# Performance work log

Measured on AMD Instinct MI355X. Metric: run time of the kernel, lower is better.

Reference implementation:

```python
import jax, jax.numpy as jnp
import numpy as np

N, M = 32768, 1024

def setup_inputs() -> dict:
    key = jax.random.key(0)
    k1, k2, k3, k4, k5 = jax.random.split(key, 5)
    origins = jax.random.normal(k1, (N, 2), dtype=jnp.float32)
    directions = jax.random.normal(k2, (N, 2), dtype=jnp.float32)
    means = jax.random.normal(k3, (M, 4), dtype=jnp.float32)
    # SPD covariances: A @ A^T + I so the inverse is well-defined
    A = jax.random.normal(k4, (M, 4, 4), dtype=jnp.float32) * 0.5
    covariances = jnp.einsum('mij,mkj->mik', A, A) + jnp.eye(4, dtype=jnp.float32)
    labels_embedding = jax.random.normal(k5, (M,), dtype=jnp.float32)
    return {"origins": origins, "directions": directions, "means": means,
            "covariances": covariances, "labels_embedding": labels_embedding}

def reference(origins, directions, means, covariances, labels_embedding):
    pos = jnp.concatenate([origins, directions], axis=1)          # [N,4]
    Sigma_inv = jnp.linalg.inv(covariances)                       # [M,4,4]
    diffs = pos[:, None, :] - means[None, :, :]                   # [N,M,4]
    quad = jnp.einsum('nmd,mde,nme->nm', diffs, Sigma_inv, diffs)  # [N,M]
    pdf = jnp.exp(-0.5 * quad) * labels_embedding[None, :]        # [N,M]
    prob = jax.nn.sigmoid(jnp.sum(pdf, axis=1))                   # [N]
    return prob.reshape(-1, 1)
```

## Files before the change

### kernel.cpp

```cpp
#include <hip/hip_runtime.h>
#include <hip/hip_bf16.h>
#include <math.h>

#define N_RAYS  32768
#define M_GAUSS 1024

typedef short v8s __attribute__((ext_vector_type(8)));
typedef float v4f __attribute__((ext_vector_type(4)));

__device__ __forceinline__ float fexp2(float x) {
#if __has_builtin(__builtin_amdgcn_exp2f)
    return __builtin_amdgcn_exp2f(x);
#else
    return exp2f(x);
#endif
}

union BFU { __hip_bfloat16 b; unsigned short u; };
__device__ __forceinline__ unsigned short f2bf(float f) { BFU x; x.b = __float2bfloat16(f); return x.u; }
__device__ __forceinline__ float bf2f(unsigned short u)  { BFU x; x.u = u; return __bfloat162float(x.b); }

__device__ __forceinline__ void split_bf16(float f, unsigned short& hi, unsigned short& lo) {
    hi = f2bf(f);
    lo = f2bf(f - bf2f(hi));
}

__device__ __forceinline__ void store8(unsigned short* dst, const unsigned short* s) {
    uint4 v;
    v.x = (unsigned)s[0] | ((unsigned)s[1] << 16);
    v.y = (unsigned)s[2] | ((unsigned)s[3] << 16);
    v.z = (unsigned)s[4] | ((unsigned)s[5] << 16);
    v.w = (unsigned)s[6] | ((unsigned)s[7] << 16);
    *reinterpret_cast<uint4*>(dst) = v;
}

__global__ __launch_bounds__(256) void prep_kernel(
    const float*  __restrict__ means,
    const float*  __restrict__ covs,
    unsigned short* __restrict__ Bt)
{
    const int g = blockIdx.x * 256 + threadIdx.x;
    if (g >= M_GAUSS) return;

    const float4* C4 = reinterpret_cast<const float4*>(covs + 16 * g);
    const float4 r0 = C4[0], r1 = C4[1], r2 = C4[2], r3 = C4[3];
    const float a00=r0.x, a01=r0.y, a02=r0.z, a03=r0.w;
    const float a10=r1.x, a11=r1.y, a12=r1.z, a13=r1.w;
    const float a20=r2.x, a21=r2.y, a22=r2.z, a23=r2.w;
    const float a30=r3.x, a31=r3.y, a32=r3.z, a33=r3.w;

    const float s0=a00*a11-a01*a10, s1=a00*a12-a02*a10, s2=a00*a13-a03*a10;
    const float s3=a01*a12-a02*a11, s4=a01*a13-a03*a11, s5=a02*a13-a03*a12;
    const float c5=a22*a33-a23*a32, c4=a21*a33-a23*a31, c3=a21*a32-a22*a31;
    const float c2=a20*a33-a23*a30, c1=a20*a32-a22*a30, c0=a20*a31-a21*a30;
    const float det = s0*c5 - s1*c4 + s2*c3 + s3*c2 - s4*c1 + s5*c0;
    const float id  = 1.0f / det;

    const float b00=( a11*c5 - a12*c4 + a13*c3)*id;
    const float b01=(-a01*c5 + a02*c4 - a03*c3)*id;
    const float b10=(-a10*c5 + a12*c2 - a13*c1)*id;
    const float b11=( a00*c5 - a02*c2 + a03*c1)*id;
    const float b20=( a10*c4 - a11*c2 + a13*c0)*id;
    const float b21=(-a00*c4 + a01*c2 - a03*c0)*id;
    const float b30=(-a10*c3 + a11*c1 - a12*c0)*id;
    const float b31=( a00*c3 - a01*c1 + a02*c0)*id;
    const float b02=( a31*s5 - a32*s4 + a33*s3)*id;
    const float b03=(-a21*s5 + a22*s4 - a23*s3)*id;
    const float b12=(-a30*s5 + a32*s2 - a33*s1)*id;
    const float b13=( a20*s5 - a22*s2 + a23*s1)*id;
    const float b22=( a30*s4 - a31*s2 + a33*s0)*id;
    const float b23=(-a20*s4 + a21*s2 - a23*s0)*id;
    const float b32=(-a30*s3 + a31*s1 - a32*s0)*id;
    const float b33=( a20*s3 - a21*s1 + a22*s0)*id;

    const float m01=0.5f*(b01+b10), m02=0.5f*(b02+b20), m03=0.5f*(b03+b30);
    const float m12=0.5f*(b12+b21), m13=0.5f*(b13+b31), m23=0.5f*(b23+b32);

    const float4 mu = reinterpret_cast<const float4*>(means)[g];
    const float u0=mu.x, u1=mu.y, u2=mu.z, u3=mu.w;
    const float v0 = b00*u0 + m01*u1 + m02*u2 + m03*u3;
    const float v1 = m01*u0 + b11*u1 + m12*u2 + m13*u3;
    const float v2 = m02*u0 + m12*u1 + b22*u2 + m23*u3;
    const float v3 = m03*u0 + m13*u1 + m23*u2 + b33*u3;
    const float cc = u0*v0 + u1*v1 + u2*v2 + u3*v3;

    const float k  = -0.72134752044448170368f;
    const float k2 = 2.0f * k;
    float w[16] = { k*b00,  k*b11,  k*b22,  k*b33,
                    k2*m01, k2*m02, k2*m03, k2*m12, k2*m13, k2*m23,
                    -k2*v0, -k2*v1, -k2*v2, -k2*v3, k*cc, 0.0f };
    unsigned short whi[16], wlo[16];
    #pragma unroll
    for (int q = 0; q < 16; ++q) split_bf16(w[q], whi[q], wlo[q]);

    const int t = g >> 4, cg = g & 15;
    unsigned short* b1 = Bt + (size_t)t * 32 * 8;
    store8(b1 + (0*16 + cg) * 8, whi + 0);
    store8(b1 + (1*16 + cg) * 8, whi + 8);
    unsigned short* b2 = Bt + (size_t)2048 * 8 + (size_t)t * 32 * 8;
    store8(b2 + (0*16 + cg) * 8, wlo + 0);
    store8(b2 + (1*16 + cg) * 8, wlo + 8);
}

__global__ __launch_bounds__(512) void decoder_kernel(
    const float2* __restrict__ org,
    const float2* __restrict__ dir,
    const uint4* __restrict__ Btg,
    const float* __restrict__ labels,
    float*       __restrict__ out)
{
    __shared__ uint4 lds[4096 + 256];

    const int tid = threadIdx.x;
    const int L   = tid & 63;
    const int w   = tid >> 6;
    const int c15 = L & 15;
    const int q   = L >> 4;

    #pragma unroll
    for (int i = 0; i < 8; ++i) lds[i * 512 + tid] = Btg[i * 512 + tid];

    if (tid < 64) {
        const int ray = blockIdx.x * 64 + tid;
        const float2 o = org[ray];
        const float2 d = dir[ray];
        const float p0 = o.x, p1 = o.y, p2 = d.x, p3 = d.y;
        float f[16] = { p0*p0, p1*p1, p2*p2, p3*p3,
                        p0*p1, p0*p2, p0*p3, p1*p2, p1*p3, p2*p3,
                        p0, p1, p2, p3, 1.0f, 0.0f };
        unsigned short hi[16], lo[16];
        #pragma unroll
        for (int k = 0; k < 16; ++k) split_bf16(f[k], hi[k], lo[k]);

        unsigned short* At = reinterpret_cast<unsigned short*>(lds + 4096);
        const int rt = tid >> 4, c = tid & 15;
        unsigned short* base = At + rt * 64 * 8;
        store8(base + (0*16 + c) * 8, hi + 0);
        store8(base + (1*16 + c) * 8, hi + 8);
        store8(base + (2*16 + c) * 8, lo + 0);
        store8(base + (3*16 + c) * 8, lo + 8);
    }
    __syncthreads();

    v8s af[4];
    #pragma unroll
    for (int rt = 0; rt < 4; ++rt) {
        union { uint4 u; v8s s; } x;
        x.u = lds[4096 + rt * 64 + L];
        af[rt] = x.s;
    }

    v4f acc[4];
    #pragma unroll
    for (int rt = 0; rt < 4; ++rt) acc[rt] = (v4f){0.f, 0.f, 0.f, 0.f};

    const bool loHalf = (L < 32);
    #pragma unroll
    for (int i = 0; i < 8; ++i) {
        const int t = w * 8 + i;
        union { uint4 u; v8s s; } b1x, b2x;
        b1x.u = lds[t * 32 + (L & 31)];
        uint4 b2u = lds[2048 + t * 32 + (L & 31)];
        if (!loHalf) { b2u.x = 0; b2u.y = 0; b2u.z = 0; b2u.w = 0; }
        b2x.u = b2u;
        const float lab = labels[t * 16 + c15];

        #pragma unroll
        for (int rt = 0; rt < 4; ++rt) {
            v4f cz = (v4f){0.f, 0.f, 0.f, 0.f};
            v4f s = __builtin_amdgcn_mfma_f32_16x16x32_bf16(af[rt], b2x.s, cz, 0, 0, 0);
            s = __builtin_amdgcn_mfma_f32_16x16x32_bf16(af[rt], b1x.s, s, 0, 0, 0);
            #pragma unroll
            for (int r = 0; r < 4; ++r)
                acc[rt][r] = fmaf(lab, fexp2(s[r]), acc[rt][r]);
        }
    }

    __syncthreads();
    float* P = reinterpret_cast<float*>(lds);
    #pragma unroll
    for (int rt = 0; rt < 4; ++rt) {
        #pragma unroll
        for (int r = 0; r < 4; ++r) {
            const int ray = rt * 16 + q * 4 + r;
            P[(w << 10) + (ray << 4) + c15] = acc[rt][r];
        }
    }
    __syncthreads();

    if (tid < 64) {
        float tsum = 0.f;
        #pragma unroll
        for (int wv = 0; wv < 8; ++wv) {
            const float4* row = reinterpret_cast<const float4*>(P + (wv << 10) + (tid << 4));
            #pragma unroll
            for (int c4 = 0; c4 < 4; ++c4) {
                const float4 v = row[c4];
                tsum += (v.x + v.y) + (v.z + v.w);
            }
        }
        const float e = fexp2(-tsum * 1.4426950408889634f);
        out[blockIdx.x * 64 + tid] = 1.0f / (1.0f + e);
    }
}

extern "C" void kernel_launch(void* const* d_in, const int* in_sizes, int n_in,
                              void* d_out, int out_size, void* d_ws, size_t ws_size,
                              hipStream_t stream) {
    const float* origins    = (const float*)d_in[0];
    const float* directions = (const float*)d_in[1];
    const float* means      = (const float*)d_in[2];
    const float* covs       = (const float*)d_in[3];
    const float* labels     = (const float*)d_in[4];
    float* out = (float*)d_out;

    unsigned short* Bt = (unsigned short*)d_ws;

    prep_kernel<<<dim3(M_GAUSS / 256), dim3(256), 0, stream>>>(means, covs, Bt);
    decoder_kernel<<<dim3(N_RAYS / 64), dim3(512), 0, stream>>>(
        (const float2*)origins, (const float2*)directions,
        (const uint4*)Bt, labels, out);
}
```

Measured before the change: 70.71 us.

## Drop LDS staging, stream Gaussian tiles from global and shuffle-reduce

The decoder no longer copies the 64 KB Gaussian weight table into LDS per block. Each wave now owns one 16-ray tile and half of the Gaussians, builds its bf16 hi/lo A fragments in registers, and reads B tiles directly from global/L2. Partial sums are reduced with xor shuffles, and only a tiny LDS array combines the two halves. This removes the large LDS footprint and the staging barriers so more blocks fit per CU (launch bounds 512,4). The cost is repeated global loads of the B table with no reuse across row tiles. The prep kernel is also split into more, smaller blocks.

```diff
diff --git a/kernel.cpp b/kernel.cpp
--- a/kernel.cpp
+++ b/kernel.cpp
@@ -34,12 +34,12 @@
     *reinterpret_cast<uint4*>(dst) = v;
 }
 
-__global__ __launch_bounds__(256) void prep_kernel(
+__global__ __launch_bounds__(64) void prep_kernel(
     const float*  __restrict__ means,
     const float*  __restrict__ covs,
     unsigned short* __restrict__ Bt)
 {
-    const int g = blockIdx.x * 256 + threadIdx.x;
+    const int g = blockIdx.x * 64 + threadIdx.x;
     if (g >= M_GAUSS) return;
 
     const float4* C4 = reinterpret_cast<const float4*>(covs + 16 * g);
@@ -102,104 +102,107 @@
     store8(b2 + (1*16 + cg) * 8, wlo + 8);
 }
 
-__global__ __launch_bounds__(512) void decoder_kernel(
+__global__ __launch_bounds__(512, 4) void decoder_kernel(
     const float2* __restrict__ org,
     const float2* __restrict__ dir,
     const uint4* __restrict__ Btg,
     const float* __restrict__ labels,
     float*       __restrict__ out)
 {
-    __shared__ uint4 lds[4096 + 256];
+    __shared__ float P[2 * 64];
 
     const int tid = threadIdx.x;
     const int L   = tid & 63;
     const int w   = tid >> 6;
     const int c15 = L & 15;
     const int q   = L >> 4;
-
+    const int rt  = w & 3;
+    const int h   = w >> 2;
+
+    const int ray = blockIdx.x * 64 + rt * 16 + c15;
+    const float2 o = org[ray];
+    const float2 d = dir[ray];
+    const float p0 = o.x, p1 = o.y, p2 = d.x, p3 = d.y;
+
+    const float f0 = p0*p0, f1 = p1*p1, f2 = p2*p2, f3 = p3*p3;
+    const float f4 = p0*p1, f5 = p0*p2, f6 = p0*p3, f7 = p1*p2;
+    const float f8 = p1*p3, f9 = p2*p3, f10 = p0,  f11 = p1;
+    const float f12 = p2,  f13 = p3,  f14 = 1.0f,  f15 = 0.0f;
+
+    const bool k8  = (q & 1) != 0;
+    const bool loQ = (q >> 1) != 0;
+
+    float g[8];
+    g[0] = k8 ? f8  : f0;
+    g[1] = k8 ? f9  : f1;
+    g[2] = k8 ? f10 : f2;
+    g[3] = k8 ? f11 : f3;
+    g[4] = k8 ? f12 : f4;
+    g[5] = k8 ? f13 : f5;
+    g[6] = k8 ? f14 : f6;
+    g[7] = k8 ? f15 : f7;
+
+    unsigned short va[8], va2[8];
     #pragma unroll
-    for (int i = 0; i < 8; ++i) lds[i * 512 + tid] = Btg[i * 512 + tid];
+    for (int j = 0; j < 8; ++j) {
+        unsigned short hi, lo;
+        split_bf16(g[j], hi, lo);
+        va[j]  = loQ ? lo : hi;
+        va2[j] = loQ ? (unsigned short)0 : hi;
+    }
+    union { uint4 u; v8s s; } afu, af2u;
+    afu.u.x  = (unsigned)va[0]  | ((unsigned)va[1]  << 16);
+    afu.u.y  = (unsigned)va[2]  | ((unsigned)va[3]  << 16);
+    afu.u.z  = (unsigned)va[4]  | ((unsigned)va[5]  << 16);
+    afu.u.w  = (unsigned)va[6]  | ((unsigned)va[7]  << 16);
+    af2u.u.x = (unsigned)va2[0] | ((unsigned)va2[1] << 16);
+    af2u.u.y = (unsigned)va2[2] | ((unsigned)va2[3] << 16);
+    af2u.u.z = (unsigned)va2[4] | ((unsigned)va2[5] << 16);
+    af2u.u.w = (unsigned)va2[6] | ((unsigned)va2[7] << 16);
+    const v8s af  = afu.s;
+    const v8s af2 = af2u.s;
+
+    const uint4* B1 = Btg;
+    const uint4* B2 = Btg + 2048;
+    const int l31 = L & 31;
+
+    v4f acc = (v4f){0.f, 0.f, 0.f, 0.f};
+    #pragma unroll 8
+    for (int i = 0; i < 32; ++i) {
+        const int t = h * 32 + i;
+        union { uint4 u; v8s s; } b1x, b2x;
+        b1x.u = B1[t * 32 + l31];
+        b2x.u = B2[t * 32 + l31];
+        const float lab = labels[t * 16 + c15];
+
+        v4f s = __builtin_amdgcn_mfma_f32_16x16x32_bf16(
+                    af2, b2x.s, (v4f){0.f, 0.f, 0.f, 0.f}, 0, 0, 0);
+        s = __builtin_amdgcn_mfma_f32_16x16x32_bf16(af, b1x.s, s, 0, 0, 0);
+
+        #pragma unroll
+        for (int r = 0; r < 4; ++r)
+            acc[r] = fmaf(lab, fexp2(s[r]), acc[r]);
+    }
+
+    float s0 = acc[0], s1 = acc[1], s2 = acc[2], s3 = acc[3];
+    #pragma unroll
+    for (int m = 1; m < 16; m <<= 1) {
+        s0 += __shfl_xor(s0, m);
+        s1 += __shfl_xor(s1, m);
+        s2 += __shfl_xor(s2, m);
+        s3 += __shfl_xor(s3, m);
+    }
+    float val = s0;
+    val = (c15 == 1) ? s1 : val;
+    val = (c15 == 2) ? s2 : val;
+    val = (c15 == 3) ? s3 : val;
+    if (c15 < 4) P[h * 64 + rt * 16 + q * 4 + c15] = val;
+
+    __syncthreads();
 
     if (tid < 64) {
-        const int ray = blockIdx.x * 64 + tid;
-        const float2 o = org[ray];
-        const float2 d = dir[ray];
-        const float p0 = o.x, p1 = o.y, p2 = d.x, p3 = d.y;
-        float f[16] = { p0*p0, p1*p1, p2*p2, p3*p3,
-                        p0*p1, p0*p2, p0*p3, p1*p2, p1*p3, p2*p3,
-                        p0, p1, p2, p3, 1.0f, 0.0f };
-        unsigned short hi[16], lo[16];
-        #pragma unroll
-        for (int k = 0; k < 16; ++k) split_bf16(f[k], hi[k], lo[k]);
-
-        unsigned short* At = reinterpret_cast<unsigned short*>(lds + 4096);
-        const int rt = tid >> 4, c = tid & 15;
-        unsigned short* base = At + rt * 64 * 8;
-        store8(base + (0*16 + c) * 8, hi + 0);
-        store8(base + (1*16 + c) * 8, hi + 8);
-        store8(base + (2*16 + c) * 8, lo + 0);
-        store8(base + (3*16 + c) * 8, lo + 8);
-    }
-    __syncthreads();
-
-    v8s af[4];
-    #pragma unroll
-    for (int rt = 0; rt < 4; ++rt) {
-        union { uint4 u; v8s s; } x;
-        x.u = lds[4096 + rt * 64 + L];
-        af[rt] = x.s;
-    }
-
-    v4f acc[4];
-    #pragma unroll
-    for (int rt = 0; rt < 4; ++rt) acc[rt] = (v4f){0.f, 0.f, 0.f, 0.f};
-
-    const bool loHalf = (L < 32);
-    #pragma unroll
-    for (int i = 0; i < 8; ++i) {
-        const int t = w * 8 + i;
-        union { uint4 u; v8s s; } b1x, b2x;
-        b1x.u = lds[t * 32 + (L & 31)];
-        uint4 b2u = lds[2048 + t * 32 + (L & 31)];
-        if (!loHalf) { b2u.x = 0; b2u.y = 0; b2u.z = 0; b2u.w = 0; }
-        b2x.u = b2u;
-        const float lab = labels[t * 16 + c15];
-
-        #pragma unroll
-        for (int rt = 0; rt < 4; ++rt) {
-            v4f cz = (v4f){0.f, 0.f, 0.f, 0.f};
-            v4f s = __builtin_amdgcn_mfma_f32_16x16x32_bf16(af[rt], b2x.s, cz, 0, 0, 0);
-            s = __builtin_amdgcn_mfma_f32_16x16x32_bf16(af[rt], b1x.s, s, 0, 0, 0);
-            #pragma unroll
-            for (int r = 0; r < 4; ++r)
-                acc[rt][r] = fmaf(lab, fexp2(s[r]), acc[rt][r]);
-        }
-    }
-
-    __syncthreads();
-    float* P = reinterpret_cast<float*>(lds);
-    #pragma unroll
-    for (int rt = 0; rt < 4; ++rt) {
-        #pragma unroll
-        for (int r = 0; r < 4; ++r) {
-            const int ray = rt * 16 + q * 4 + r;
-            P[(w << 10) + (ray << 4) + c15] = acc[rt][r];
-        }
-    }
-    __syncthreads();
-
-    if (tid < 64) {
-        float tsum = 0.f;
-        #pragma unroll
-        for (int wv = 0; wv < 8; ++wv) {
-            const float4* row = reinterpret_cast<const float4*>(P + (wv << 10) + (tid << 4));
-            #pragma unroll
-            for (int c4 = 0; c4 < 4; ++c4) {
-                const float4 v = row[c4];
-                tsum += (v.x + v.y) + (v.z + v.w);
-            }
-        }
-        const float e = fexp2(-tsum * 1.4426950408889634f);
+        const float ts = P[tid] + P[64 + tid];
+        const float e = fexp2(-ts * 1.4426950408889634f);
         out[blockIdx.x * 64 + tid] = 1.0f / (1.0f + e);
     }
 }
@@ -216,7 +219,7 @@
 
     unsigned short* Bt = (unsigned short*)d_ws;
 
-    prep_kernel<<<dim3(M_GAUSS / 256), dim3(256), 0, stream>>>(means, covs, Bt);
+    prep_kernel<<<dim3(M_GAUSS / 64), dim3(64), 0, stream>>>(means, covs, Bt);
     decoder_kernel<<<dim3(N_RAYS / 64), dim3(512), 0, stream>>>(
         (const float2*)origins, (const float2*)directions,
         (const uint4*)Bt, labels, out);
```

Result: slower. 72.30 us (+2.2%).
